# Kernel tuning notes

Measured on AMD Instinct MI355X. Metric: run time of the kernel, lower is better.

The kernel has to match this reference:

```python
import jax, jax.numpy as jnp
import numpy as np

EPS = 6.4 / 255.0  # HistoGAN EPS
H_BINS = 64
SIGMA = 0.02


def rgb_uv_hist(x):
    """Differentiable RGB-uv histogram, x: [B,3,H,W] in [0,1]. Returns [B,3,h,h]."""
    x = jnp.clip(x, 0.0, 1.0)
    B = x.shape[0]
    I = x.reshape(B, 3, -1).transpose(0, 2, 1)  # [B, N, 3]
    Iy = jnp.sqrt(jnp.sum(I * I, axis=-1) + EPS)  # [B, N] intensity scale
    logI = jnp.log(I + EPS)  # [B, N, 3]
    delta = jnp.linspace(-3.0, 3.0, H_BINS, dtype=x.dtype)  # bin centers [h]

    def kernel(d):
        # inverse-quadratic: 1 / (1 + (|d - delta| / sigma)^2), d: [B,N] -> [B,N,h]
        diff = jnp.abs(d[..., None] - delta)
        return 1.0 / (1.0 + (diff * diff) / (SIGMA * SIGMA))

    # channel c uses u = log(c) - log(other1), v = log(c) - log(other2)
    chans = [(0, 1, 2), (1, 0, 2), (2, 0, 1)]
    hists = []
    for c, o1, o2 in chans:
        ku = kernel(logI[..., c] - logI[..., o1])  # [B,N,h]
        kv = kernel(logI[..., c] - logI[..., o2])  # [B,N,h]
        a = Iy[..., None] * ku  # [B,N,h]
        hists.append(jnp.einsum('bnu,bnv->buv', a, kv))  # [B,h,h]
    hists = jnp.stack(hists, axis=1)  # [B,3,h,h]
    norm = jnp.sum(hists, axis=(1, 2, 3), keepdims=True) + EPS
    return hists / norm


def setup_inputs() -> dict:
    key = jax.random.key(0)
    k1, k2 = jax.random.split(key)
    rgbd = jax.random.normal(k1, (8, 4, 256, 256), dtype=jnp.float32)
    th = jax.random.uniform(k2, (3, 64, 64), dtype=jnp.float32)
    th = th / jnp.sum(th)  # target histogram is a normalized distribution
    return {"rgbd": rgbd, "target_hist": th}


def reference(rgbd, target_hist):
    rgb = 0.5 * (rgbd[:, 0:3, :, :] + 1.0)
    hist = rgb_uv_hist(rgb)  # [B,3,64,64]
    # Hellinger-style histogram loss (HistoGAN histogram_loss)
    d = jnp.sqrt(target_hist) - jnp.sqrt(hist)
    loss = (1.0 / jnp.sqrt(2.0)) * jnp.sqrt(jnp.sum(d * d)) / hist.shape[0]
    return loss
```

## Files before the change

kernel.cpp:

```cpp
#include <hip/hip_runtime.h>
#include <hip/hip_bf16.h>
#include <math.h>

#define NPIX 65536
#define SEGB 32
#define HEPS (6.4f / 255.0f)

typedef __bf16 bf16x8 __attribute__((ext_vector_type(8)));
typedef float  f32x4  __attribute__((ext_vector_type(4)));

__device__ __forceinline__ float clamp01(float x) { return fminf(fmaxf(x, 0.f), 1.f); }

template <int PART>
__global__ __launch_bounds__(512) void hist_mfma(const float* __restrict__ rgbd,
                                                 float* __restrict__ out) {
  const int blk = blockIdx.x;
  const int seg = blk & (SEGB - 1);
  const int bc  = blk / SEGB;
  const int b = bc / 3;
  const int c = bc - 3 * b;
  const int t = threadIdx.x;
  const int l = t & 63;
  const int w = t >> 6;

  __shared__ float stage[8][3][64];
  __shared__ float red[4096];

  const float* __restrict__ base = rgbd + (size_t)b * (4 * NPIX);

  f32x4 acc[4][4];
#pragma unroll
  for (int i = 0; i < 4; ++i)
#pragma unroll
    for (int j = 0; j < 4; ++j) acc[i][j] = (f32x4){0.f, 0.f, 0.f, 0.f};

  const int halfq = l & 15;
  const int grp   = l >> 4;
  const float d0  = -3.f + (float)halfq * (6.f / 63.f);
  const float dstep = 16.f * 6.f / 63.f;

  const int p0  = seg * (NPIX / SEGB) + w * (NPIX / SEGB / 8);
  const int NIT = (NPIX / SEGB / 8) / 64;

  float pr = base[p0 + l];
  float pg = base[NPIX + p0 + l];
  float pb = base[2 * NPIX + p0 + l];

  for (int it = 0; it < NIT; ++it) {
    float r  = clamp01(0.5f * (pr + 1.f));
    float g  = clamp01(0.5f * (pg + 1.f));
    float bl = clamp01(0.5f * (pb + 1.f));
    float iy = sqrtf(fmaf(r, r, fmaf(g, g, fmaf(bl, bl, HEPS))));
    float lr = __logf(r + HEPS);
    float lg = __logf(g + HEPS);
    float lb = __logf(bl + HEPS);
    float u, v;
    if (c == 0)      { u = lr - lg; v = lr - lb; }
    else if (c == 1) { u = lg - lr; v = lg - lb; }
    else             { u = lb - lr; v = lb - lg; }
    stage[w][0][l] = u;
    stage[w][1][l] = v;
    stage[w][2][l] = iy;

    if (it + 1 < NIT) {
      const int p = p0 + (it + 1) * 64 + l;
      pr = base[p]; pg = base[NPIX + p]; pb = base[2 * NPIX + p];
    }
    asm volatile("s_waitcnt lgkmcnt(0)" ::: "memory");

#pragma unroll
    for (int s = 0; s < 2; ++s) {
      const int k0 = s * 32 + grp * 8;
      float u8[8], iy8[8], v8[8];
      *(f32x4*)&u8[0]  = *(const f32x4*)&stage[w][0][k0];
      *(f32x4*)&u8[4]  = *(const f32x4*)&stage[w][0][k0 + 4];
      *(f32x4*)&iy8[0] = *(const f32x4*)&stage[w][2][k0];
      *(f32x4*)&iy8[4] = *(const f32x4*)&stage[w][2][k0 + 4];

      bf16x8 af[4];
#pragma unroll
      for (int ut = 0; ut < 4; ++ut) {
        const float dlt = d0 + (float)ut * dstep;
#pragma unroll
        for (int j = 0; j < 8; ++j) {
          const float du = u8[j] - dlt;
          const float x  = du * 50.f;
          const float q  = fmaf(x, x, 1.f);
          af[ut][j] = (__bf16)(iy8[j] * __builtin_amdgcn_rcpf(q));
        }
      }

      *(f32x4*)&v8[0] = *(const f32x4*)&stage[w][1][k0];
      *(f32x4*)&v8[4] = *(const f32x4*)&stage[w][1][k0 + 4];

#pragma unroll
      for (int vt = 0; vt < 4; ++vt) {
        const float dlt = d0 + (float)vt * dstep;
        bf16x8 bf;
#pragma unroll
        for (int j = 0; j < 8; ++j) {
          const float dv = v8[j] - dlt;
          const float x  = dv * 50.f;
          const float q  = fmaf(x, x, 1.f);
          bf[j] = (__bf16)__builtin_amdgcn_rcpf(q);
        }
#pragma unroll
        for (int ut = 0; ut < 4; ++ut)
          acc[ut][vt] = __builtin_amdgcn_mfma_f32_16x16x32_bf16(af[ut], bf, acc[ut][vt], 0, 0, 0);
      }
    }
  }

  for (int ww = 0; ww < 8; ++ww) {
    if (w == ww) {
#pragma unroll
      for (int ut = 0; ut < 4; ++ut)
#pragma unroll
        for (int vt = 0; vt < 4; ++vt)
#pragma unroll
          for (int rg = 0; rg < 4; ++rg) {
            const int row = ut * 16 + grp * 4 + rg;
            const int col = vt * 16 + halfq;
            if (ww == 0) red[row * 64 + col]  = acc[ut][vt][rg];
            else         red[row * 64 + col] += acc[ut][vt][rg];
          }
    }
    __syncthreads();
  }

  if (PART) {
    float* __restrict__ P = out + (size_t)blk * 4096;
    for (int i = t; i < 4096; i += 512) P[i] = red[i];
  } else {
    float* __restrict__ Hbc = out + (size_t)bc * 4096;
    for (int i = t; i < 4096; i += 512) atomicAdd(&Hbc[i], red[i]);
  }
}

__global__ __launch_bounds__(256) void reduce_partials(float* __restrict__ P,
                                                       float* __restrict__ norms) {
  const int e   = blockIdx.x * 256 + threadIdx.x;
  const int bc  = e >> 12;
  const int bin = e & 4095;
  float* __restrict__ p0 = P + (size_t)(bc * SEGB) * 4096 + bin;
  float s = 0.f;
#pragma unroll
  for (int sg = 0; sg < SEGB; ++sg) s += p0[(size_t)sg * 4096];
  p0[0] = s;

  __shared__ float red[4];
  float ns = s;
#pragma unroll
  for (int off = 32; off > 0; off >>= 1) ns += __shfl_down(ns, off);
  if ((threadIdx.x & 63) == 0) red[threadIdx.x >> 6] = ns;
  __syncthreads();
  if (threadIdx.x == 0)
    atomicAdd(&norms[bc / 3], red[0] + red[1] + red[2] + red[3]);
}

__global__ __launch_bounds__(256) void loss_partials(const float* __restrict__ P,
                                                     const float* __restrict__ norms,
                                                     const float* __restrict__ th,
                                                     float* __restrict__ acc) {
  float s = 0.f;
  for (int idx = blockIdx.x * 256 + threadIdx.x; idx < 8 * 12288;
       idx += gridDim.x * 256) {
    const int b   = idx / 12288;
    const int r   = idx - b * 12288;
    const int c   = r >> 12;
    const int bin = r & 4095;
    const float h = P[(size_t)((b * 3 + c) * SEGB) * 4096 + bin] / (norms[b] + HEPS);
    const float d = sqrtf(th[r]) - sqrtf(h);
    s += d * d;
  }
  __shared__ float red[4];
#pragma unroll
  for (int off = 32; off > 0; off >>= 1) s += __shfl_down(s, off);
  if ((threadIdx.x & 63) == 0) red[threadIdx.x >> 6] = s;
  __syncthreads();
  if (threadIdx.x == 0) atomicAdd(acc, red[0] + red[1] + red[2] + red[3]);
}

__global__ __launch_bounds__(256) void norm_kernel(const float* __restrict__ H,
                                                   float* __restrict__ norms) {
  const int b = blockIdx.x;
  const float* __restrict__ Hb = H + b * 12288;
  float s = 0.f;
  for (int i = threadIdx.x; i < 12288; i += 256) s += Hb[i];
  __shared__ float red[4];
#pragma unroll
  for (int off = 32; off > 0; off >>= 1) s += __shfl_down(s, off);
  if ((threadIdx.x & 63) == 0) red[threadIdx.x >> 6] = s;
  __syncthreads();
  if (threadIdx.x == 0) norms[b] = red[0] + red[1] + red[2] + red[3] + HEPS;
}

__global__ __launch_bounds__(256) void loss_kernel(const float* __restrict__ H,
                                                   const float* __restrict__ norms,
                                                   const float* __restrict__ th,
                                                   float* __restrict__ acc) {
  float s = 0.f;
  for (int idx = blockIdx.x * 256 + threadIdx.x; idx < 8 * 12288;
       idx += gridDim.x * 256) {
    const int b = idx / 12288;
    const int r = idx - b * 12288;
    const float h = H[idx] / norms[b];
    const float d = sqrtf(th[r]) - sqrtf(h);
    s += d * d;
  }
  __shared__ float red[4];
#pragma unroll
  for (int off = 32; off > 0; off >>= 1) s += __shfl_down(s, off);
  if ((threadIdx.x & 63) == 0) red[threadIdx.x >> 6] = s;
  __syncthreads();
  if (threadIdx.x == 0) atomicAdd(acc, red[0] + red[1] + red[2] + red[3]);
}

__global__ void final_kernel(const float* __restrict__ acc, float* __restrict__ out) {
  out[0] = sqrtf(acc[0]) * 0.08838834764831845f;
}

extern "C" void kernel_launch(void* const* d_in, const int* in_sizes, int n_in,
                              void* d_out, int out_size, void* d_ws, size_t ws_size,
                              hipStream_t stream) {
  const float* rgbd = (const float*)d_in[0];
  const float* th   = (const float*)d_in[1];
  float* out = (float*)d_out;

  const size_t nP = (size_t)24 * SEGB * 4096;
  if (ws_size >= (nP + 64) * sizeof(float)) {
    float* P     = (float*)d_ws;
    float* norms = P + nP;
    float* acc   = norms + 8;
    hipMemsetAsync(norms, 0, 16 * sizeof(float), stream);
    hist_mfma<1><<<24 * SEGB, 512, 0, stream>>>(rgbd, P);
    reduce_partials<<<384, 256, 0, stream>>>(P, norms);
    loss_partials<<<96, 256, 0, stream>>>(P, norms, th, acc);
    final_kernel<<<1, 1, 0, stream>>>(acc, out);
  } else {
    float* H     = (float*)d_ws;
    float* norms = H + 24 * 4096;
    float* acc   = norms + 8;
    hipMemsetAsync(d_ws, 0, (size_t)(24 * 4096 + 16) * sizeof(float), stream);
    hist_mfma<0><<<24 * SEGB, 512, 0, stream>>>(rgbd, H);
    norm_kernel<<<8, 256, 0, stream>>>(H, norms);
    loss_kernel<<<96, 256, 0, stream>>>(H, norms, th, acc);
    final_kernel<<<1, 1, 0, stream>>>(acc, out);
  }
}
```

Before: 129.0 us.

## Shrink histogram blocks, store MFMA fragments directly, fuse final loss kernel

```diff
diff --git a/kernel.cpp b/kernel.cpp
--- a/kernel.cpp
+++ b/kernel.cpp
@@ -8,12 +8,13 @@
 
 typedef __bf16 bf16x8 __attribute__((ext_vector_type(8)));
 typedef float  f32x4  __attribute__((ext_vector_type(4)));
+typedef float  f32x2  __attribute__((ext_vector_type(2)));
 
 __device__ __forceinline__ float clamp01(float x) { return fminf(fmaxf(x, 0.f), 1.f); }
 
-template <int PART>
-__global__ __launch_bounds__(512) void hist_mfma(const float* __restrict__ rgbd,
-                                                 float* __restrict__ out) {
+__global__ __launch_bounds__(256) void hist_mfma(const float* __restrict__ rgbd,
+                                                 float* __restrict__ P,
+                                                 float* __restrict__ ctrl) {
   const int blk = blockIdx.x;
   const int seg = blk & (SEGB - 1);
   const int bc  = blk / SEGB;
@@ -23,33 +24,33 @@
   const int l = t & 63;
   const int w = t >> 6;
 
-  __shared__ float stage[8][3][64];
-  __shared__ float red[4096];
+  if (blk == 0 && t < 16) ctrl[t] = 0.f;
+
+  __shared__ float stage[4][3][64];
+  __shared__ f32x4 slab[2][16][64];
 
   const float* __restrict__ base = rgbd + (size_t)b * (4 * NPIX);
 
-  f32x4 acc[4][4];
-#pragma unroll
-  for (int i = 0; i < 4; ++i)
-#pragma unroll
-    for (int j = 0; j < 4; ++j) acc[i][j] = (f32x4){0.f, 0.f, 0.f, 0.f};
+  f32x4 acc[16];
+#pragma unroll
+  for (int i = 0; i < 16; ++i) acc[i] = (f32x4){0.f, 0.f, 0.f, 0.f};
 
   const int halfq = l & 15;
   const int grp   = l >> 4;
-  const float d0  = -3.f + (float)halfq * (6.f / 63.f);
-  const float dstep = 16.f * 6.f / 63.f;
-
-  const int p0  = seg * (NPIX / SEGB) + w * (NPIX / SEGB / 8);
-  const int NIT = (NPIX / SEGB / 8) / 64;
+  const float d50_0   = (-3.f + (float)halfq * (6.f / 63.f)) * 50.f;
+  const float dstep50 = (16.f * 6.f / 63.f) * 50.f;
+  const f32x2 one2 = {1.f, 1.f};
+
+  const int p0 = seg * 2048 + w * 512;
 
   float pr = base[p0 + l];
   float pg = base[NPIX + p0 + l];
   float pb = base[2 * NPIX + p0 + l];
 
-  for (int it = 0; it < NIT; ++it) {
-    float r  = clamp01(0.5f * (pr + 1.f));
-    float g  = clamp01(0.5f * (pg + 1.f));
-    float bl = clamp01(0.5f * (pb + 1.f));
+  for (int it = 0; it < 8; ++it) {
+    float r  = clamp01(fmaf(pr, 0.5f, 0.5f));
+    float g  = clamp01(fmaf(pg, 0.5f, 0.5f));
+    float bl = clamp01(fmaf(pb, 0.5f, 0.5f));
     float iy = sqrtf(fmaf(r, r, fmaf(g, g, fmaf(bl, bl, HEPS))));
     float lr = __logf(r + HEPS);
     float lg = __logf(g + HEPS);
@@ -58,11 +59,11 @@
     if (c == 0)      { u = lr - lg; v = lr - lb; }
     else if (c == 1) { u = lg - lr; v = lg - lb; }
     else             { u = lb - lr; v = lb - lg; }
-    stage[w][0][l] = u;
-    stage[w][1][l] = v;
+    stage[w][0][l] = u * 50.f;
+    stage[w][1][l] = v * 50.f;
     stage[w][2][l] = iy;
 
-    if (it + 1 < NIT) {
+    if (it + 1 < 8) {
       const int p = p0 + (it + 1) * 64 + l;
       pr = base[p]; pg = base[NPIX + p]; pb = base[2 * NPIX + p];
     }
@@ -71,78 +72,74 @@
 #pragma unroll
     for (int s = 0; s < 2; ++s) {
       const int k0 = s * 32 + grp * 8;
-      float u8[8], iy8[8], v8[8];
-      *(f32x4*)&u8[0]  = *(const f32x4*)&stage[w][0][k0];
-      *(f32x4*)&u8[4]  = *(const f32x4*)&stage[w][0][k0 + 4];
-      *(f32x4*)&iy8[0] = *(const f32x4*)&stage[w][2][k0];
-      *(f32x4*)&iy8[4] = *(const f32x4*)&stage[w][2][k0 + 4];
+      const f32x2* __restrict__ u2  = (const f32x2*)&stage[w][0][k0];
+      const f32x2* __restrict__ v2  = (const f32x2*)&stage[w][1][k0];
+      const f32x2* __restrict__ iy2 = (const f32x2*)&stage[w][2][k0];
 
       bf16x8 af[4];
 #pragma unroll
       for (int ut = 0; ut < 4; ++ut) {
-        const float dlt = d0 + (float)ut * dstep;
-#pragma unroll
-        for (int j = 0; j < 8; ++j) {
-          const float du = u8[j] - dlt;
-          const float x  = du * 50.f;
-          const float q  = fmaf(x, x, 1.f);
-          af[ut][j] = (__bf16)(iy8[j] * __builtin_amdgcn_rcpf(q));
+        const float dlt = d50_0 + (float)ut * dstep50;
+        const f32x2 dlt2 = {dlt, dlt};
+#pragma unroll
+        for (int jp = 0; jp < 4; ++jp) {
+          f32x2 x = u2[jp] - dlt2;
+          f32x2 q = x * x + one2;
+          f32x2 rc = {__builtin_amdgcn_rcpf(q[0]), __builtin_amdgcn_rcpf(q[1])};
+          f32x2 a2 = iy2[jp] * rc;
+          af[ut][2 * jp]     = (__bf16)a2[0];
+          af[ut][2 * jp + 1] = (__bf16)a2[1];
         }
       }
 
-      *(f32x4*)&v8[0] = *(const f32x4*)&stage[w][1][k0];
-      *(f32x4*)&v8[4] = *(const f32x4*)&stage[w][1][k0 + 4];
-
 #pragma unroll
       for (int vt = 0; vt < 4; ++vt) {
-        const float dlt = d0 + (float)vt * dstep;
+        const float dlt = d50_0 + (float)vt * dstep50;
+        const f32x2 dlt2 = {dlt, dlt};
         bf16x8 bf;
 #pragma unroll
-        for (int j = 0; j < 8; ++j) {
-          const float dv = v8[j] - dlt;
-          const float x  = dv * 50.f;
-          const float q  = fmaf(x, x, 1.f);
-          bf[j] = (__bf16)__builtin_amdgcn_rcpf(q);
+        for (int jp = 0; jp < 4; ++jp) {
+          f32x2 x = v2[jp] - dlt2;
+          f32x2 q = x * x + one2;
+          bf[2 * jp]     = (__bf16)__builtin_amdgcn_rcpf(q[0]);
+          bf[2 * jp + 1] = (__bf16)__builtin_amdgcn_rcpf(q[1]);
         }
 #pragma unroll
         for (int ut = 0; ut < 4; ++ut)
-          acc[ut][vt] = __builtin_amdgcn_mfma_f32_16x16x32_bf16(af[ut], bf, acc[ut][vt], 0, 0, 0);
+          acc[ut * 4 + vt] =
+              __builtin_amdgcn_mfma_f32_16x16x32_bf16(af[ut], bf, acc[ut * 4 + vt], 0, 0, 0);
       }
     }
   }
 
-  for (int ww = 0; ww < 8; ++ww) {
-    if (w == ww) {
-#pragma unroll
-      for (int ut = 0; ut < 4; ++ut)
-#pragma unroll
-        for (int vt = 0; vt < 4; ++vt)
-#pragma unroll
-          for (int rg = 0; rg < 4; ++rg) {
-            const int row = ut * 16 + grp * 4 + rg;
-            const int col = vt * 16 + halfq;
-            if (ww == 0) red[row * 64 + col]  = acc[ut][vt][rg];
-            else         red[row * 64 + col] += acc[ut][vt][rg];
-          }
-    }
-    __syncthreads();
-  }
-
-  if (PART) {
-    float* __restrict__ P = out + (size_t)blk * 4096;
-    for (int i = t; i < 4096; i += 512) P[i] = red[i];
-  } else {
-    float* __restrict__ Hbc = out + (size_t)bc * 4096;
-    for (int i = t; i < 4096; i += 512) atomicAdd(&Hbc[i], red[i]);
+  if (w >= 2) {
+#pragma unroll
+    for (int i = 0; i < 16; ++i) slab[w - 2][i][l] = acc[i];
+  }
+  __syncthreads();
+  if (w < 2) {
+#pragma unroll
+    for (int i = 0; i < 16; ++i) acc[i] += slab[w][i][l];
+  }
+  __syncthreads();
+  if (w == 1) {
+#pragma unroll
+    for (int i = 0; i < 16; ++i) slab[0][i][l] = acc[i];
+  }
+  __syncthreads();
+  if (w == 0) {
+    f32x4* __restrict__ Pv = (f32x4*)(P + (size_t)blk * 4096);
+#pragma unroll
+    for (int i = 0; i < 16; ++i) Pv[i * 64 + l] = acc[i] + slab[0][i][l];
   }
 }
 
 __global__ __launch_bounds__(256) void reduce_partials(float* __restrict__ P,
                                                        float* __restrict__ norms) {
-  const int e   = blockIdx.x * 256 + threadIdx.x;
-  const int bc  = e >> 12;
-  const int bin = e & 4095;
-  float* __restrict__ p0 = P + (size_t)(bc * SEGB) * 4096 + bin;
+  const int e  = blockIdx.x * 256 + threadIdx.x;
+  const int bc = e >> 12;
+  const int si = e & 4095;
+  float* __restrict__ p0 = P + (size_t)(bc * SEGB) * 4096 + si;
   float s = 0.f;
 #pragma unroll
   for (int sg = 0; sg < SEGB; ++sg) s += p0[(size_t)sg * 4096];
@@ -158,19 +155,27 @@
     atomicAdd(&norms[bc / 3], red[0] + red[1] + red[2] + red[3]);
 }
 
-__global__ __launch_bounds__(256) void loss_partials(const float* __restrict__ P,
-                                                     const float* __restrict__ norms,
-                                                     const float* __restrict__ th,
-                                                     float* __restrict__ acc) {
+__global__ __launch_bounds__(256) void loss_final(const float* __restrict__ P,
+                                                  const float* __restrict__ norms,
+                                                  const float* __restrict__ th,
+                                                  float* __restrict__ acc,
+                                                  unsigned* __restrict__ counter,
+                                                  float* __restrict__ out) {
   float s = 0.f;
   for (int idx = blockIdx.x * 256 + threadIdx.x; idx < 8 * 12288;
        idx += gridDim.x * 256) {
-    const int b   = idx / 12288;
-    const int r   = idx - b * 12288;
-    const int c   = r >> 12;
-    const int bin = r & 4095;
-    const float h = P[(size_t)((b * 3 + c) * SEGB) * 4096 + bin] / (norms[b] + HEPS);
-    const float d = sqrtf(th[r]) - sqrtf(h);
+    const int b  = idx / 12288;
+    const int r  = idx - b * 12288;
+    const int c  = r >> 12;
+    const int si = r & 4095;
+    const int rg = si & 3;
+    const int q  = si >> 2;
+    const int l  = q & 63;
+    const int i  = q >> 6;
+    const int row = (i >> 2) * 16 + (l >> 4) * 4 + rg;
+    const int col = (i & 3) * 16 + (l & 15);
+    const float h = P[(size_t)((b * 3 + c) * SEGB) * 4096 + si] / (norms[b] + HEPS);
+    const float d = sqrtf(th[c * 4096 + row * 64 + col]) - sqrtf(h);
     s += d * d;
   }
   __shared__ float red[4];
@@ -178,46 +183,15 @@
   for (int off = 32; off > 0; off >>= 1) s += __shfl_down(s, off);
   if ((threadIdx.x & 63) == 0) red[threadIdx.x >> 6] = s;
   __syncthreads();
-  if (threadIdx.x == 0) atomicAdd(acc, red[0] + red[1] + red[2] + red[3]);
-}
-
-__global__ __launch_bounds__(256) void norm_kernel(const float* __restrict__ H,
-                                                   float* __restrict__ norms) {
-  const int b = blockIdx.x;
-  const float* __restrict__ Hb = H + b * 12288;
-  float s = 0.f;
-  for (int i = threadIdx.x; i < 12288; i += 256) s += Hb[i];
-  __shared__ float red[4];
-#pragma unroll
-  for (int off = 32; off > 0; off >>= 1) s += __shfl_down(s, off);
-  if ((threadIdx.x & 63) == 0) red[threadIdx.x >> 6] = s;
-  __syncthreads();
-  if (threadIdx.x == 0) norms[b] = red[0] + red[1] + red[2] + red[3] + HEPS;
-}
-
-__global__ __launch_bounds__(256) void loss_kernel(const float* __restrict__ H,
-                                                   const float* __restrict__ norms,
-                                                   const float* __restrict__ th,
-                                                   float* __restrict__ acc) {
-  float s = 0.f;
-  for (int idx = blockIdx.x * 256 + threadIdx.x; idx < 8 * 12288;
-       idx += gridDim.x * 256) {
-    const int b = idx / 12288;
-    const int r = idx - b * 12288;
-    const float h = H[idx] / norms[b];
-    const float d = sqrtf(th[r]) - sqrtf(h);
-    s += d * d;
-  }
-  __shared__ float red[4];
-#pragma unroll
-  for (int off = 32; off > 0; off >>= 1) s += __shfl_down(s, off);
-  if ((threadIdx.x & 63) == 0) red[threadIdx.x >> 6] = s;
-  __syncthreads();
-  if (threadIdx.x == 0) atomicAdd(acc, red[0] + red[1] + red[2] + red[3]);
-}
-
-__global__ void final_kernel(const float* __restrict__ acc, float* __restrict__ out) {
-  out[0] = sqrtf(acc[0]) * 0.08838834764831845f;
+  if (threadIdx.x == 0) {
+    atomicAdd(acc, red[0] + red[1] + red[2] + red[3]);
+    __threadfence();
+    const unsigned old = atomicAdd(counter, 1u);
+    if (old == (unsigned)(gridDim.x - 1)) {
+      const float tot = atomicAdd(acc, 0.f);
+      out[0] = sqrtf(tot) * 0.08838834764831845f;
+    }
+  }
 }
 
 extern "C" void kernel_launch(void* const* d_in, const int* in_sizes, int n_in,
@@ -228,23 +202,13 @@
   float* out = (float*)d_out;
 
   const size_t nP = (size_t)24 * SEGB * 4096;
-  if (ws_size >= (nP + 64) * sizeof(float)) {
-    float* P     = (float*)d_ws;
-    float* norms = P + nP;
-    float* acc   = norms + 8;
-    hipMemsetAsync(norms, 0, 16 * sizeof(float), stream);
-    hist_mfma<1><<<24 * SEGB, 512, 0, stream>>>(rgbd, P);
-    reduce_partials<<<384, 256, 0, stream>>>(P, norms);
-    loss_partials<<<96, 256, 0, stream>>>(P, norms, th, acc);
-    final_kernel<<<1, 1, 0, stream>>>(acc, out);
-  } else {
-    float* H     = (float*)d_ws;
-    float* norms = H + 24 * 4096;
-    float* acc   = norms + 8;
-    hipMemsetAsync(d_ws, 0, (size_t)(24 * 4096 + 16) * sizeof(float), stream);
-    hist_mfma<0><<<24 * SEGB, 512, 0, stream>>>(rgbd, H);
-    norm_kernel<<<8, 256, 0, stream>>>(H, norms);
-    loss_kernel<<<96, 256, 0, stream>>>(H, norms, th, acc);
-    final_kernel<<<1, 1, 0, stream>>>(acc, out);
-  }
-}
+  float*    P       = (float*)d_ws;
+  float*    ctrl    = P + nP;
+  float*    norms   = ctrl;
+  float*    acc     = ctrl + 8;
+  unsigned* counter = (unsigned*)(ctrl + 9);
+
+  hist_mfma<<<24 * SEGB, 256, 0, stream>>>(rgbd, P, ctrl);
+  reduce_partials<<<384, 256, 0, stream>>>(P, norms);
+  loss_final<<<96, 256, 0, stream>>>(P, norms, th, acc, counter, out);
+}
```

Result: faster. 108.7 us (-15.8%).
